# Kernel tuning notes

Measured on AMD Instinct MI355X. Metric: run time of the kernel, lower is better.

The kernel has to match this reference:

```python
import jax, jax.numpy as jnp
import numpy as np
from jax import lax

N_STATES = 512
VOCAB = 32000
BATCH = 16
SEQ_LEN = 128


def setup_inputs() -> dict:
    key = jax.random.key(0)
    k_ids, k_em, k_tm, k_p = jax.random.split(key, 4)
    input_ids = jax.random.randint(k_ids, (BATCH, SEQ_LEN), 0, VOCAB, dtype=jnp.int64)
    em = jax.random.normal(k_em, (N_STATES, VOCAB), dtype=jnp.float32)
    tm = jax.random.normal(k_tm, (N_STATES, N_STATES), dtype=jnp.float32)
    p = jax.random.normal(k_p, (N_STATES,), dtype=jnp.float32)
    return {"input_ids": input_ids, "em": em, "tm": tm, "p": p}


def reference(input_ids, em, tm, p):
    """HMM forward algorithm in log space; returns mean NLL (scalar).

    em: [S, V] emission logits, tm: [S, S] transition logits, p: [S] prior logits.
    do_log_softmax=True -> normalize each in log space first.
    """
    log_em = jax.nn.log_softmax(em, axis=-1)   # [S, V]
    log_tm = jax.nn.log_softmax(tm, axis=-1)   # [S, S] rows = source state
    log_p = jax.nn.log_softmax(p, axis=-1)     # [S]

    # Gather emission log-probs per token: [B, T, S]
    em_tok = log_em.T[input_ids]

    # alpha_0[b, s] = log_p[s] + log_em[s, x_0]
    alpha0 = log_p[None, :] + em_tok[:, 0]     # [B, S]

    def step(alpha, e_t):
        # alpha: [B, S_src]; log-matmul: logsumexp over source states
        a = jax.nn.logsumexp(alpha[:, :, None] + log_tm[None, :, :], axis=1) + e_t
        return a, None

    em_rest = jnp.swapaxes(em_tok[:, 1:], 0, 1)  # [T-1, B, S]
    alpha_T, _ = lax.scan(step, alpha0, em_rest)

    # loss = -mean_b log p(x_b) = -mean_b logsumexp_s alpha_T[b, s]
    loss = -jnp.mean(jax.nn.logsumexp(alpha_T, axis=-1))
    return loss
```

## Files before the change

### kernel.cpp

```cpp
#include <hip/hip_runtime.h>
#include <hip/hip_bf16.h>

#define NS 512
#define NV 32000
#define NB 16
#define NT 128

#ifndef __has_builtin
#define __has_builtin(x) 0
#endif

typedef int v8i __attribute__((ext_vector_type(8)));
typedef float v4f __attribute__((ext_vector_type(4)));

__device__ inline unsigned enc_e4m3(float x) {
    x = fminf(x, 448.0f);
    unsigned u = __float_as_uint(x);
    if (x < 0.015625f) {
        return (unsigned)(int)rintf(x * 512.0f);
    }
    unsigned u2 = u + 0x7FFFFu + ((u >> 20) & 1u);
    return (((u2 >> 23) - 120u) << 3) | ((u2 >> 20) & 7u);
}

__device__ inline unsigned pack4_e4m3(float a, float b, float c, float d) {
#if __has_builtin(__builtin_amdgcn_cvt_pk_fp8_f32)
    int v = __builtin_amdgcn_cvt_pk_fp8_f32(a, b, 0, false);
    v = __builtin_amdgcn_cvt_pk_fp8_f32(c, d, v, true);
    return (unsigned)v;
#else
    return enc_e4m3(a) | (enc_e4m3(b) << 8) | (enc_e4m3(c) << 16) | (enc_e4m3(d) << 24);
#endif
}

__device__ inline unsigned pack1_e4m3(float a) {
#if __has_builtin(__builtin_amdgcn_cvt_pk_fp8_f32)
    return (unsigned)__builtin_amdgcn_cvt_pk_fp8_f32(a, 0.f, 0, false) & 0xFFFFu;
#else
    return enc_e4m3(a);
#endif
}

#define DPPMAX(x, ctrl) \
    x = fmaxf(x, __int_as_float(__builtin_amdgcn_mov_dpp(__float_as_int(x), ctrl, 0xF, 0xF, true)))
#define DPPADD(x, ctrl) \
    x = x + __int_as_float(__builtin_amdgcn_mov_dpp(__float_as_int(x), ctrl, 0xF, 0xF, true))

#define UMX(a, b) ((a) > (b) ? (a) : (b))

__device__ inline unsigned bytemax8(unsigned a, unsigned b) {
    unsigned m0 = UMX(a & 255u, b & 255u);
    unsigned m1 = UMX((a >> 8) & 255u, (b >> 8) & 255u);
    unsigned m2 = UMX((a >> 16) & 255u, (b >> 16) & 255u);
    unsigned m3 = UMX(a >> 24, b >> 24);
    return UMX(UMX(m0, m1), UMX(m2, m3));
}

__global__ __launch_bounds__(256) void k_emtok_T(
    const float* __restrict__ em, const int* __restrict__ ids,
    float* __restrict__ em_lin_T)
{
    const int s   = blockIdx.x;
    const int tid = threadIdx.x;
    const float* row = em + (size_t)s * NV;

    int idv[8];
#pragma unroll
    for (int k = 0; k < 8; ++k) idv[k] = ids[tid + 256 * k];
    float g[8];
#pragma unroll
    for (int k = 0; k < 8; ++k) g[k] = row[idv[k]];

    float sum = 0.f;
    const float4* row4 = (const float4*)row;
#pragma unroll 4
    for (int i = 0; i < 31; ++i) {
        float4 v = row4[tid + 256 * i];
        sum += __expf(v.x) + __expf(v.y) + __expf(v.z) + __expf(v.w);
    }
    sum += __expf(row[31744 + tid]);

#pragma unroll
    for (int off = 32; off; off >>= 1) sum += __shfl_down(sum, off);
    __shared__ float red[4];
    __shared__ float s_scale;
    if ((tid & 63) == 0) red[tid >> 6] = sum;
    __syncthreads();
    if (tid == 0) s_scale = (1.0f / ((red[0] + red[1]) + (red[2] + red[3]))) * 0x1p-18f;
    __syncthreads();
    const float scale = s_scale;

#pragma unroll
    for (int k = 0; k < 8; ++k)
        em_lin_T[(size_t)s * (NB * NT) + tid + 256 * k] = __expf(g[k]) * scale;
}

__global__ __launch_bounds__(256) void k_tr(
    const float* __restrict__ emT, float* __restrict__ em_lin)
{
    __shared__ float tile[32][33];
    const int jb = blockIdx.x * 32;
    const int sb = blockIdx.y * 32;
    const int cc = threadIdx.x & 31;
    const int rr = threadIdx.x >> 5;
#pragma unroll
    for (int i = 0; i < 4; ++i) {
        int r = rr + 8 * i;
        tile[r][cc] = emT[(size_t)(sb + r) * (NB * NT) + jb + cc];
    }
    __syncthreads();
#pragma unroll
    for (int i = 0; i < 4; ++i) {
        int r = rr + 8 * i;
        int s = sb + cc;
        int ps = (s & ~63) | ((s & 15) << 2) | ((s >> 4) & 3);
        em_lin[(size_t)(jb + r) * NS + ps] = tile[cc][r];
    }
}

__global__ __launch_bounds__(64) void k_z(
    const float* __restrict__ tm, float* __restrict__ zscale)
{
    const int k    = blockIdx.x;
    const int lane = threadIdx.x;
    const float* row = tm + (size_t)k * NS;

    float4 a = ((const float4*)row)[lane * 2];
    float4 b = ((const float4*)row)[lane * 2 + 1];
    float sum = ((__expf(a.x) + __expf(a.y)) + (__expf(a.z) + __expf(a.w)))
              + ((__expf(b.x) + __expf(b.y)) + (__expf(b.z) + __expf(b.w)));
#pragma unroll
    for (int off = 32; off; off >>= 1) sum += __shfl_down(sum, off);
    if (lane == 0) zscale[k] = 1024.0f / sum;
}

__global__ __launch_bounds__(256) void k_pt2(
    const float* __restrict__ tm, const float* __restrict__ zscale,
    unsigned char* __restrict__ PT)
{
    __shared__ float tile[64][65];
    __shared__ float zs[64];
    const int kb  = blockIdx.x * 64;
    const int db  = blockIdx.y * 64;
    const int tid = threadIdx.x;
    const int c   = tid & 63;
    const int r0  = tid >> 6;

    if (tid < 64) zs[tid] = zscale[kb + tid];
#pragma unroll
    for (int i = 0; i < 16; ++i) {
        int r = r0 + 4 * i;
        tile[r][c] = tm[(size_t)(kb + r) * NS + db + c];
    }
    __syncthreads();

    const int d  = tid >> 2;
    const int ks = (tid & 3) * 16;
    unsigned px[4];
#pragma unroll
    for (int gq = 0; gq < 4; ++gq) {
        int k0 = ks + gq * 4;
        px[gq] = pack4_e4m3(__expf(tile[k0 + 0][d]) * zs[k0 + 0],
                            __expf(tile[k0 + 1][d]) * zs[k0 + 1],
                            __expf(tile[k0 + 2][d]) * zs[k0 + 2],
                            __expf(tile[k0 + 3][d]) * zs[k0 + 3]);
    }
    uint4 o; o.x = px[0]; o.y = px[1]; o.z = px[2]; o.w = px[3];
    *(uint4*)(PT + (size_t)(db + d) * NS + kb + ks) = o;
}

__global__ __launch_bounds__(512, 2) void k_scan(
    const float* __restrict__ em_lin, const unsigned char* __restrict__ PT,
    const float* __restrict__ p, float* __restrict__ out)
{
    const int bb  = blockIdx.x;
    const int tid = threadIdx.x;
    const int w   = tid >> 6;
    const int l   = tid & 63;
    const int lc  = l & 15;
    const int lq  = l >> 4;

    __shared__ __align__(16) unsigned Ew[2][16 * 128];
    __shared__ __align__(4) unsigned char wmE2[2][32];
    __shared__ __align__(4) unsigned char mbuf[2][4];
    __shared__ float    wm2[8][4];
    __shared__ float    sbuf[4];

    v8i B[4][4];
#pragma unroll
    for (int nt = 0; nt < 4; ++nt) {
#pragma unroll
        for (int kt = 0; kt < 4; ++kt) {
            const uint4* src = (const uint4*)(PT + (size_t)((w * 4 + nt) * 16 + lc) * NS + kt * 128 + lq * 32);
            v8i bb8;
            *(uint4*)&bb8       = src[0];
            *((uint4*)&bb8 + 1) = src[1];
            B[nt][kt] = bb8;
        }
    }

    {
        uint4 zz; zz.x = 0; zz.y = 0; zz.z = 0; zz.w = 0;
        uint4* z = (uint4*)&Ew[0][0];
        z[tid * 2]     = zz;
        z[tid * 2 + 1] = zz;
    }

    float zp = 0.f;
#pragma unroll
    for (int i = 0; i < 8; ++i) zp += __expf(p[l * 8 + i]);
    DPPADD(zp, 0x128); DPPADD(zp, 0x124); DPPADD(zp, 0xB1); DPPADD(zp, 0x4E);
    float Zp = __int_as_float(__builtin_amdgcn_readlane(__float_as_int(zp), 0))
             + __int_as_float(__builtin_amdgcn_readlane(__float_as_int(zp), 16))
             + __int_as_float(__builtin_amdgcn_readlane(__float_as_int(zp), 32))
             + __int_as_float(__builtin_amdgcn_readlane(__float_as_int(zp), 48));
    const float invZp = 1.0f / Zp;

    const int dbase0 = w * 64 + lc;
    const int gb     = bb * 4 + lq;

    const float* epb0 = em_lin + (size_t)gb * (NT * NS) + (w * 64 + lc * 4);
    v4f e0 = *(const v4f*)epb0;
    float alpha[4];
#pragma unroll
    for (int nt = 0; nt < 4; ++nt)
        alpha[nt] = __expf(p[dbase0 + 16 * nt]) * invZp * e0[nt];

    int gsum = 18;
    const unsigned sel1 = (l & 1) ? 0x07030501u : 0x02060004u;
    const unsigned sel2 = (l & 2) ? 0x07060302u : 0x01000504u;
    const int mrow = 4 * lq + (l & 3);

    int aidx[8];
#pragma unroll
    for (int kt = 0; kt < 4; ++kt) {
#pragma unroll
        for (int c = 0; c < 2; ++c)
            aidx[kt * 2 + c] = lc * 32 + (((kt * 8 + lq * 2 + c) ^ lc) & 31);
    }
    int widx[4];
#pragma unroll
    for (int nt = 0; nt < 4; ++nt)
        widx[nt] = mrow * 128 + ((((w * 4 + nt) ^ mrow) & 31) << 2) + (lc >> 2);

    const int bA = lc >> 2;
    const int h  = lq >> 1;
    const int wexp_w = (w & 1) * 16 + lq * 4 + (w >> 1);
    const int wexp_r = h * 16 + bA * 4;
    const unsigned shA = (unsigned)(bA << 3);
    const unsigned shQ = (unsigned)(lq << 3);
    const bool real = (l & 3) == 0;

    const float* epb = epb0 + NS;

    {
        float mx = fmaxf(fmaxf(alpha[0], alpha[1]), fmaxf(alpha[2], alpha[3]));
        DPPMAX(mx, 0x128); DPPMAX(mx, 0x124); DPPMAX(mx, 0xB1); DPPMAX(mx, 0x4E);
        unsigned E = __float_as_uint(mx) >> 23;
        E = E > 1u ? E : 1u;
        if (lc == 0) wmE2[1][wexp_w] = (unsigned char)E;
    }
    __syncthreads();
    if (tid < 4) {
        const unsigned u0 = *(const unsigned*)&wmE2[1][tid * 4];
        const unsigned u1 = *(const unsigned*)&wmE2[1][16 + tid * 4];
        mbuf[1][tid] = (unsigned char)bytemax8(u0, u1);
    }

    const v4f CZ = {0.f, 0.f, 0.f, 0.f};

    v8i A[4];
#pragma unroll
    for (int kt = 0; kt < 4; ++kt)
#pragma unroll
        for (int i = 0; i < 8; ++i) A[kt][i] = 0;

    for (int t = 1; t < NT; ++t) {
        const int buf = t & 1;
        unsigned* EwB = &Ew[buf][0];

        float mx = fmaxf(fmaxf(alpha[0], alpha[1]), fmaxf(alpha[2], alpha[3]));
        DPPMAX(mx, 0x128); DPPMAX(mx, 0x124); DPPMAX(mx, 0xB1); DPPMAX(mx, 0x4E);
        unsigned E = __float_as_uint(mx) >> 23;
        E = E > 1u ? E : 1u;
        const float sc = __uint_as_float((261u - E) << 23);

        unsigned dwv[4];
#pragma unroll
        for (int nt = 0; nt < 4; ++nt) {
            unsigned dw = pack1_e4m3(alpha[nt] * sc);
            int tmp = __builtin_amdgcn_mov_dpp((int)dw, 0xB1, 0xF, 0xF, true);
            dw = __builtin_amdgcn_perm(dw, (unsigned)tmp, sel1);
            tmp = __builtin_amdgcn_mov_dpp((int)dw, 0x4E, 0xF, 0xF, true);
            dw = __builtin_amdgcn_perm(dw, (unsigned)tmp, sel2);
            dwv[nt] = dw;
        }
        if (real) {
#pragma unroll
            for (int nt = 0; nt < 4; ++nt) EwB[widx[nt]] = dwv[nt];
        }
        if (lc == 0) wmE2[buf][wexp_w] = (unsigned char)E;
        __syncthreads();

        v4f epf = *(const v4f*)epb;
        epb += NS;

        if (real) {
            const uint4* eb4 = (const uint4*)EwB;
#pragma unroll
            for (int kt = 0; kt < 4; ++kt) {
                *(uint4*)&A[kt]       = eb4[aidx[kt * 2 + 0]];
                *((uint4*)&A[kt] + 1) = eb4[aidx[kt * 2 + 1]];
            }
        }

        if (tid < 4) {
            const unsigned u0 = *(const unsigned*)&wmE2[buf][tid * 4];
            const unsigned u1 = *(const unsigned*)&wmE2[buf][16 + tid * 4];
            mbuf[buf ^ 1][tid] = (unsigned char)bytemax8(u0, u1);
        }

        const unsigned mdw = *(const unsigned*)&mbuf[buf][0];
        const int MhA = (int)((mdw >> shA) & 255u);
        const int MhQ = (int)((mdw >> shQ) & 255u);
        gsum += MhQ - 126;

        const unsigned dwE = *(const unsigned*)&wmE2[buf][wexp_r];
        const int base = 127 - MhA;
        int s0 = (int)(dwE & 255u) + base;         s0 = s0 < 0 ? 0 : (s0 > 254 ? 254 : s0);
        int s1 = (int)((dwE >> 8) & 255u) + base;  s1 = s1 < 0 ? 0 : (s1 > 254 ? 254 : s1);
        int s2 = (int)((dwE >> 16) & 255u) + base; s2 = s2 < 0 ? 0 : (s2 > 254 ? 254 : s2);
        int s3 = (int)(dwE >> 24) + base;          s3 = s3 < 0 ? 0 : (s3 > 254 ? 254 : s3);
        const int scA[4] = { s0 * 0x01010101, s1 * 0x01010101,
                             s2 * 0x01010101, s3 * 0x01010101 };

        v4f Ca[4], Cb[4];
#pragma unroll
        for (int nt = 0; nt < 4; ++nt) {
            Ca[nt] = __builtin_amdgcn_mfma_scale_f32_16x16x128_f8f6f4(
                         A[0], B[nt][0], CZ, 0, 0, 0, scA[0], 0, 0x7F7F7F7F);
            Cb[nt] = __builtin_amdgcn_mfma_scale_f32_16x16x128_f8f6f4(
                         A[2], B[nt][2], CZ, 0, 0, 0, scA[2], 0, 0x7F7F7F7F);
        }
#pragma unroll
        for (int nt = 0; nt < 4; ++nt) {
            Ca[nt] = __builtin_amdgcn_mfma_scale_f32_16x16x128_f8f6f4(
                         A[1], B[nt][1], Ca[nt], 0, 0, 0, scA[1], 0, 0x7F7F7F7F);
            Cb[nt] = __builtin_amdgcn_mfma_scale_f32_16x16x128_f8f6f4(
                         A[3], B[nt][3], Cb[nt], 0, 0, 0, scA[3], 0, 0x7F7F7F7F);
        }

#pragma unroll
        for (int nt = 0; nt < 4; ++nt)
            alpha[nt] = (Ca[nt][0] + Cb[nt][0]) * epf[nt];
    }

    {
        float sm = (alpha[0] + alpha[1]) + (alpha[2] + alpha[3]);
        DPPADD(sm, 0x128); DPPADD(sm, 0x124); DPPADD(sm, 0xB1); DPPADD(sm, 0x4E);
        if (lc == 0) wm2[w][lq] = sm;
        if (w == 0 && lc == 0) sbuf[lq] = (float)gsum;
    }
    __syncthreads();
    if (tid < 4) {
        float s8 = ((wm2[0][tid] + wm2[1][tid]) + (wm2[2][tid] + wm2[3][tid]))
                 + ((wm2[4][tid] + wm2[5][tid]) + (wm2[6][tid] + wm2[7][tid]));
        float L2 = __log2f(s8) + sbuf[tid];
        atomicAdd(out, -(0.693147180559945f / 16.0f) * L2);
    }
}

extern "C" void kernel_launch(void* const* d_in, const int* in_sizes, int n_in,
                              void* d_out, int out_size, void* d_ws, size_t ws_size,
                              hipStream_t stream)
{
    const int*   ids = (const int*)d_in[0];
    const float* em  = (const float*)d_in[1];
    const float* tm  = (const float*)d_in[2];
    const float* p   = (const float*)d_in[3];
    float* out = (float*)d_out;

    float*          em_lin = (float*)d_ws;
    unsigned char*  PT     = (unsigned char*)d_ws + ((size_t)4 << 20);
    float*          zscale = (float*)((unsigned char*)d_ws + ((size_t)4 << 20) + ((size_t)256 << 10));
    float*          emT    = (float*)((unsigned char*)d_ws + ((size_t)4 << 20) + ((size_t)512 << 10));

    hipMemsetAsync(d_out, 0, sizeof(float), stream);

    k_emtok_T<<<NS, 256, 0, stream>>>(em, ids, emT);
    k_tr<<<dim3(64, 16), 256, 0, stream>>>(emT, em_lin);
    k_z<<<NS, 64, 0, stream>>>(tm, zscale);
    k_pt2<<<dim3(8, 8), 256, 0, stream>>>(tm, zscale, PT);
    k_scan<<<4, 512, 0, stream>>>(em_lin, PT, p, out);
}
```

Baseline: 249.7 us.

## Halve scan block to 4 waves, each owning 128 destination states

The sequential scan kernel drops from 8 waves of 512 threads to 4 waves of 256 threads, so each wave holds twice the transition-matrix fragments (8x4 v8i registers) and computes 8 output tiles per step. The emission layout permutation is widened to match the new 8-per-lane ordering. The per-step max-exponent reduction is restructured, and the mbuf update moves after the MFMAs so it overlaps with them. Fewer waves means cheaper barriers on the latency-bound 127-step chain, at the cost of doubling per-wave MFMA and register work.

```diff
diff --git a/kernel.cpp b/kernel.cpp
--- a/kernel.cpp
+++ b/kernel.cpp
@@ -113,7 +113,7 @@
     for (int i = 0; i < 4; ++i) {
         int r = rr + 8 * i;
         int s = sb + cc;
-        int ps = (s & ~63) | ((s & 15) << 2) | ((s >> 4) & 3);
+        int ps = (s & ~127) | ((s & 15) << 3) | ((s >> 4) & 7);
         em_lin[(size_t)(jb + r) * NS + ps] = tile[cc][r];
     }
 }
@@ -169,7 +169,7 @@
     *(uint4*)(PT + (size_t)(db + d) * NS + kb + ks) = o;
 }
 
-__global__ __launch_bounds__(512, 2) void k_scan(
+__global__ __launch_bounds__(256, 1) void k_scan(
     const float* __restrict__ em_lin, const unsigned char* __restrict__ PT,
     const float* __restrict__ p, float* __restrict__ out)
 {
@@ -181,17 +181,17 @@
     const int lq  = l >> 4;
 
     __shared__ __align__(16) unsigned Ew[2][16 * 128];
-    __shared__ __align__(4) unsigned char wmE2[2][32];
+    __shared__ __align__(4) unsigned char wmE[2][64];
     __shared__ __align__(4) unsigned char mbuf[2][4];
-    __shared__ float    wm2[8][4];
+    __shared__ float    wm2[4][4];
     __shared__ float    sbuf[4];
 
-    v8i B[4][4];
-#pragma unroll
-    for (int nt = 0; nt < 4; ++nt) {
+    v8i B[8][4];
+#pragma unroll
+    for (int nt = 0; nt < 8; ++nt) {
 #pragma unroll
         for (int kt = 0; kt < 4; ++kt) {
-            const uint4* src = (const uint4*)(PT + (size_t)((w * 4 + nt) * 16 + lc) * NS + kt * 128 + lq * 32);
+            const uint4* src = (const uint4*)(PT + (size_t)(128 * w + 16 * nt + lc) * NS + kt * 128 + lq * 32);
             v8i bb8;
             *(uint4*)&bb8       = src[0];
             *((uint4*)&bb8 + 1) = src[1];
@@ -202,8 +202,8 @@
     {
         uint4 zz; zz.x = 0; zz.y = 0; zz.z = 0; zz.w = 0;
         uint4* z = (uint4*)&Ew[0][0];
-        z[tid * 2]     = zz;
-        z[tid * 2 + 1] = zz;
+#pragma unroll
+        for (int i = 0; i < 8; ++i) z[tid + 256 * i] = zz;
     }
 
     float zp = 0.f;
@@ -216,15 +216,16 @@
              + __int_as_float(__builtin_amdgcn_readlane(__float_as_int(zp), 48));
     const float invZp = 1.0f / Zp;
 
-    const int dbase0 = w * 64 + lc;
-    const int gb     = bb * 4 + lq;
-
-    const float* epb0 = em_lin + (size_t)gb * (NT * NS) + (w * 64 + lc * 4);
-    v4f e0 = *(const v4f*)epb0;
-    float alpha[4];
-#pragma unroll
-    for (int nt = 0; nt < 4; ++nt)
-        alpha[nt] = __expf(p[dbase0 + 16 * nt]) * invZp * e0[nt];
+    const int dbase = 128 * w + lc;
+    const int gb    = bb * 4 + lq;
+
+    const float* epb0 = em_lin + (size_t)gb * (NT * NS) + (128 * w + lc * 8);
+    v4f e0a = ((const v4f*)epb0)[0];
+    v4f e0b = ((const v4f*)epb0)[1];
+    float alpha[8];
+#pragma unroll
+    for (int nt = 0; nt < 8; ++nt)
+        alpha[nt] = __expf(p[dbase + 16 * nt]) * invZp * (nt < 4 ? e0a[nt] : e0b[nt - 4]);
 
     int gsum = 18;
     const unsigned sel1 = (l & 1) ? 0x07030501u : 0x02060004u;
@@ -238,33 +239,44 @@
         for (int c = 0; c < 2; ++c)
             aidx[kt * 2 + c] = lc * 32 + (((kt * 8 + lq * 2 + c) ^ lc) & 31);
     }
-    int widx[4];
-#pragma unroll
-    for (int nt = 0; nt < 4; ++nt)
-        widx[nt] = mrow * 128 + ((((w * 4 + nt) ^ mrow) & 31) << 2) + (lc >> 2);
+    int widx[8];
+#pragma unroll
+    for (int nt = 0; nt < 8; ++nt)
+        widx[nt] = mrow * 128 + ((((8 * w + nt) ^ mrow) & 31) << 2) + (lc >> 2);
 
     const int bA = lc >> 2;
-    const int h  = lq >> 1;
-    const int wexp_w = (w & 1) * 16 + lq * 4 + (w >> 1);
-    const int wexp_r = h * 16 + bA * 4;
     const unsigned shA = (unsigned)(bA << 3);
     const unsigned shQ = (unsigned)(lq << 3);
+    const int wexp_r = (lq * 4 + bA) * 4;
     const bool real = (l & 3) == 0;
 
     const float* epb = epb0 + NS;
 
     {
-        float mx = fmaxf(fmaxf(alpha[0], alpha[1]), fmaxf(alpha[2], alpha[3]));
-        DPPMAX(mx, 0x128); DPPMAX(mx, 0x124); DPPMAX(mx, 0xB1); DPPMAX(mx, 0x4E);
-        unsigned E = __float_as_uint(mx) >> 23;
-        E = E > 1u ? E : 1u;
-        if (lc == 0) wmE2[1][wexp_w] = (unsigned char)E;
+        float m0 = fmaxf(alpha[0], alpha[1]), m1 = fmaxf(alpha[2], alpha[3]);
+        float m2 = fmaxf(alpha[4], alpha[5]), m3 = fmaxf(alpha[6], alpha[7]);
+        DPPMAX(m0, 0x128); DPPMAX(m1, 0x128); DPPMAX(m2, 0x128); DPPMAX(m3, 0x128);
+        DPPMAX(m0, 0x124); DPPMAX(m1, 0x124); DPPMAX(m2, 0x124); DPPMAX(m3, 0x124);
+        DPPMAX(m0, 0xB1);  DPPMAX(m1, 0xB1);  DPPMAX(m2, 0xB1);  DPPMAX(m3, 0xB1);
+        DPPMAX(m0, 0x4E);  DPPMAX(m1, 0x4E);  DPPMAX(m2, 0x4E);  DPPMAX(m3, 0x4E);
+        unsigned E0 = __float_as_uint(m0) >> 23; E0 = E0 > 1u ? E0 : 1u;
+        unsigned E1 = __float_as_uint(m1) >> 23; E1 = E1 > 1u ? E1 : 1u;
+        unsigned E2 = __float_as_uint(m2) >> 23; E2 = E2 > 1u ? E2 : 1u;
+        unsigned E3 = __float_as_uint(m3) >> 23; E3 = E3 > 1u ? E3 : 1u;
+        if (lc == 0) {
+            wmE[1][(0 * 4 + lq) * 4 + w] = (unsigned char)E0;
+            wmE[1][(1 * 4 + lq) * 4 + w] = (unsigned char)E1;
+            wmE[1][(2 * 4 + lq) * 4 + w] = (unsigned char)E2;
+            wmE[1][(3 * 4 + lq) * 4 + w] = (unsigned char)E3;
+        }
     }
     __syncthreads();
     if (tid < 4) {
-        const unsigned u0 = *(const unsigned*)&wmE2[1][tid * 4];
-        const unsigned u1 = *(const unsigned*)&wmE2[1][16 + tid * 4];
-        mbuf[1][tid] = (unsigned char)bytemax8(u0, u1);
+        const unsigned u0 = *(const unsigned*)&wmE[1][tid * 4];
+        const unsigned u1 = *(const unsigned*)&wmE[1][16 + tid * 4];
+        const unsigned u2 = *(const unsigned*)&wmE[1][32 + tid * 4];
+        const unsigned u3 = *(const unsigned*)&wmE[1][48 + tid * 4];
+        mbuf[1][tid] = (unsigned char)bytemax8(bytemax8(u0, u1), bytemax8(u2, u3));
     }
 
     const v4f CZ = {0.f, 0.f, 0.f, 0.f};
@@ -279,16 +291,26 @@
         const int buf = t & 1;
         unsigned* EwB = &Ew[buf][0];
 
-        float mx = fmaxf(fmaxf(alpha[0], alpha[1]), fmaxf(alpha[2], alpha[3]));
-        DPPMAX(mx, 0x128); DPPMAX(mx, 0x124); DPPMAX(mx, 0xB1); DPPMAX(mx, 0x4E);
-        unsigned E = __float_as_uint(mx) >> 23;
-        E = E > 1u ? E : 1u;
-        const float sc = __uint_as_float((261u - E) << 23);
-
-        unsigned dwv[4];
-#pragma unroll
-        for (int nt = 0; nt < 4; ++nt) {
-            unsigned dw = pack1_e4m3(alpha[nt] * sc);
+        float m0 = fmaxf(alpha[0], alpha[1]), m1 = fmaxf(alpha[2], alpha[3]);
+        float m2 = fmaxf(alpha[4], alpha[5]), m3 = fmaxf(alpha[6], alpha[7]);
+        DPPMAX(m0, 0x128); DPPMAX(m1, 0x128); DPPMAX(m2, 0x128); DPPMAX(m3, 0x128);
+        DPPMAX(m0, 0x124); DPPMAX(m1, 0x124); DPPMAX(m2, 0x124); DPPMAX(m3, 0x124);
+        DPPMAX(m0, 0xB1);  DPPMAX(m1, 0xB1);  DPPMAX(m2, 0xB1);  DPPMAX(m3, 0xB1);
+        DPPMAX(m0, 0x4E);  DPPMAX(m1, 0x4E);  DPPMAX(m2, 0x4E);  DPPMAX(m3, 0x4E);
+        unsigned Ej[4];
+        Ej[0] = __float_as_uint(m0) >> 23; Ej[0] = Ej[0] > 1u ? Ej[0] : 1u;
+        Ej[1] = __float_as_uint(m1) >> 23; Ej[1] = Ej[1] > 1u ? Ej[1] : 1u;
+        Ej[2] = __float_as_uint(m2) >> 23; Ej[2] = Ej[2] > 1u ? Ej[2] : 1u;
+        Ej[3] = __float_as_uint(m3) >> 23; Ej[3] = Ej[3] > 1u ? Ej[3] : 1u;
+        float scj[4];
+#pragma unroll
+        for (int j = 0; j < 4; ++j)
+            scj[j] = __uint_as_float((261u - Ej[j]) << 23);
+
+        unsigned dwv[8];
+#pragma unroll
+        for (int nt = 0; nt < 8; ++nt) {
+            unsigned dw = pack1_e4m3(alpha[nt] * scj[nt >> 1]);
             int tmp = __builtin_amdgcn_mov_dpp((int)dw, 0xB1, 0xF, 0xF, true);
             dw = __builtin_amdgcn_perm(dw, (unsigned)tmp, sel1);
             tmp = __builtin_amdgcn_mov_dpp((int)dw, 0x4E, 0xF, 0xF, true);
@@ -297,12 +319,21 @@
         }
         if (real) {
 #pragma unroll
-            for (int nt = 0; nt < 4; ++nt) EwB[widx[nt]] = dwv[nt];
-        }
-        if (lc == 0) wmE2[buf][wexp_w] = (unsigned char)E;
+            for (int nt = 0; nt < 8; ++nt) EwB[widx[nt]] = dwv[nt];
+        }
+        if (lc == 0) {
+            wmE[buf][(0 * 4 + lq) * 4 + w] = (unsigned char)Ej[0];
+            wmE[buf][(1 * 4 + lq) * 4 + w] = (unsigned char)Ej[1];
+            wmE[buf][(2 * 4 + lq) * 4 + w] = (unsigned char)Ej[2];
+            wmE[buf][(3 * 4 + lq) * 4 + w] = (unsigned char)Ej[3];
+        }
         __syncthreads();
 
-        v4f epf = *(const v4f*)epb;
+        const unsigned dwE = *(const unsigned*)&wmE[buf][wexp_r];
+        const unsigned mdw = *(const unsigned*)&mbuf[buf][0];
+
+        v4f epfa = ((const v4f*)epb)[0];
+        v4f epfb = ((const v4f*)epb)[1];
         epb += NS;
 
         if (real) {
@@ -314,18 +345,10 @@
             }
         }
 
-        if (tid < 4) {
-            const unsigned u0 = *(const unsigned*)&wmE2[buf][tid * 4];
-            const unsigned u1 = *(const unsigned*)&wmE2[buf][16 + tid * 4];
-            mbuf[buf ^ 1][tid] = (unsigned char)bytemax8(u0, u1);
-        }
-
-        const unsigned mdw = *(const unsigned*)&mbuf[buf][0];
         const int MhA = (int)((mdw >> shA) & 255u);
         const int MhQ = (int)((mdw >> shQ) & 255u);
         gsum += MhQ - 126;
 
-        const unsigned dwE = *(const unsigned*)&wmE2[buf][wexp_r];
         const int base = 127 - MhA;
         int s0 = (int)(dwE & 255u) + base;         s0 = s0 < 0 ? 0 : (s0 > 254 ? 254 : s0);
         int s1 = (int)((dwE >> 8) & 255u) + base;  s1 = s1 < 0 ? 0 : (s1 > 254 ? 254 : s1);
@@ -334,37 +357,41 @@
         const int scA[4] = { s0 * 0x01010101, s1 * 0x01010101,
                              s2 * 0x01010101, s3 * 0x01010101 };
 
-        v4f Ca[4], Cb[4];
-#pragma unroll
-        for (int nt = 0; nt < 4; ++nt) {
-            Ca[nt] = __builtin_amdgcn_mfma_scale_f32_16x16x128_f8f6f4(
-                         A[0], B[nt][0], CZ, 0, 0, 0, scA[0], 0, 0x7F7F7F7F);
-            Cb[nt] = __builtin_amdgcn_mfma_scale_f32_16x16x128_f8f6f4(
-                         A[2], B[nt][2], CZ, 0, 0, 0, scA[2], 0, 0x7F7F7F7F);
-        }
-#pragma unroll
-        for (int nt = 0; nt < 4; ++nt) {
-            Ca[nt] = __builtin_amdgcn_mfma_scale_f32_16x16x128_f8f6f4(
-                         A[1], B[nt][1], Ca[nt], 0, 0, 0, scA[1], 0, 0x7F7F7F7F);
-            Cb[nt] = __builtin_amdgcn_mfma_scale_f32_16x16x128_f8f6f4(
-                         A[3], B[nt][3], Cb[nt], 0, 0, 0, scA[3], 0, 0x7F7F7F7F);
-        }
-
-#pragma unroll
-        for (int nt = 0; nt < 4; ++nt)
-            alpha[nt] = (Ca[nt][0] + Cb[nt][0]) * epf[nt];
+        v4f C[8];
+#pragma unroll
+        for (int nt = 0; nt < 8; ++nt)
+            C[nt] = __builtin_amdgcn_mfma_scale_f32_16x16x128_f8f6f4(
+                        A[0], B[nt][0], CZ, 0, 0, 0, scA[0], 0, 0x7F7F7F7F);
+#pragma unroll
+        for (int kt = 1; kt < 4; ++kt)
+#pragma unroll
+            for (int nt = 0; nt < 8; ++nt)
+                C[nt] = __builtin_amdgcn_mfma_scale_f32_16x16x128_f8f6f4(
+                            A[kt], B[nt][kt], C[nt], 0, 0, 0, scA[kt], 0, 0x7F7F7F7F);
+
+        if (tid < 4) {
+            const unsigned u0 = *(const unsigned*)&wmE[buf][tid * 4];
+            const unsigned u1 = *(const unsigned*)&wmE[buf][16 + tid * 4];
+            const unsigned u2 = *(const unsigned*)&wmE[buf][32 + tid * 4];
+            const unsigned u3 = *(const unsigned*)&wmE[buf][48 + tid * 4];
+            mbuf[buf ^ 1][tid] = (unsigned char)bytemax8(bytemax8(u0, u1), bytemax8(u2, u3));
+        }
+
+#pragma unroll
+        for (int nt = 0; nt < 8; ++nt)
+            alpha[nt] = C[nt][0] * (nt < 4 ? epfa[nt] : epfb[nt - 4]);
     }
 
     {
-        float sm = (alpha[0] + alpha[1]) + (alpha[2] + alpha[3]);
+        float sm = ((alpha[0] + alpha[1]) + (alpha[2] + alpha[3]))
+                 + ((alpha[4] + alpha[5]) + (alpha[6] + alpha[7]));
         DPPADD(sm, 0x128); DPPADD(sm, 0x124); DPPADD(sm, 0xB1); DPPADD(sm, 0x4E);
         if (lc == 0) wm2[w][lq] = sm;
         if (w == 0 && lc == 0) sbuf[lq] = (float)gsum;
     }
     __syncthreads();
     if (tid < 4) {
-        float s8 = ((wm2[0][tid] + wm2[1][tid]) + (wm2[2][tid] + wm2[3][tid]))
-                 + ((wm2[4][tid] + wm2[5][tid]) + (wm2[6][tid] + wm2[7][tid]));
+        float s8 = (wm2[0][tid] + wm2[1][tid]) + (wm2[2][tid] + wm2[3][tid]);
         float L2 = __log2f(s8) + sbuf[tid];
         atomicAdd(out, -(0.693147180559945f / 16.0f) * L2);
     }
@@ -391,5 +418,5 @@
     k_tr<<<dim3(64, 16), 256, 0, stream>>>(emT, em_lin);
     k_z<<<NS, 64, 0, stream>>>(tm, zscale);
     k_pt2<<<dim3(8, 8), 256, 0, stream>>>(tm, zscale, PT);
-    k_scan<<<4, 512, 0, stream>>>(em_lin, PT, p, out);
-}
+    k_scan<<<4, 256, 0, stream>>>(em_lin, PT, p, out);
+}
```

New measurement: 271.0 us. 8.5% more time.
